# Kernel tuning notes

Hardware: AMD Instinct MI355X
Metric: run time of the kernel (lower is better)

## Reference

```python
import jax, jax.numpy as jnp
import numpy as np

D_MODEL, H, KV, D = 2048, 32, 8, 64
G = H // KV  # groups = 4
B, T = 1, 2048


def rotate_half(x):
    # interleaved rotation: (-x1, x0, -x3, x2, ...)
    x_even = x[..., ::2]
    x_odd = x[..., 1::2]
    return jnp.stack((-x_odd, x_even), axis=-1).reshape(x.shape)


def setup_inputs() -> dict:
    key = jax.random.key(0)
    kx, kq, kk, kv, ko = jax.random.split(key, 5)
    x = jax.random.normal(kx, (B, T, D_MODEL), dtype=jnp.float32)
    # RoPE frequency table: freqs[0]=cos, freqs[1]=sin, each [T, D] with pairwise-repeated angles
    inv_freq = 1.0 / (10000.0 ** (jnp.arange(0, D, 2, dtype=jnp.float32) / D))  # [D/2]
    angles = jnp.arange(T, dtype=jnp.float32)[:, None] * inv_freq[None, :]       # [T, D/2]
    angles = jnp.repeat(angles, 2, axis=-1)                                       # [T, D]
    freqs = jnp.stack((jnp.cos(angles), jnp.sin(angles)), axis=0)                 # [2, T, D]
    # causal mask, broadcastable to [B, H, T, T]
    mask = jnp.tril(jnp.ones((T, T), dtype=bool))[None, None]
    s = 0.02
    Wq = s * jax.random.normal(kq, (D_MODEL, H * D), dtype=jnp.float32)
    Wk = s * jax.random.normal(kk, (D_MODEL, KV * D), dtype=jnp.float32)
    Wv = s * jax.random.normal(kv, (D_MODEL, KV * D), dtype=jnp.float32)
    Wo = s * jax.random.normal(ko, (D_MODEL, D_MODEL), dtype=jnp.float32)
    return {"x": x, "freqs": freqs, "mask": mask, "Wq": Wq, "Wk": Wk, "Wv": Wv, "Wo": Wo}


def reference(x, freqs, mask, Wq, Wk, Wv, Wo):
    b, t, _ = x.shape
    Q = (x @ Wq).reshape(b, t, H, D)
    K = (x @ Wk).reshape(b, t, KV, D)
    V = (x @ Wv).reshape(b, t, KV, D)
    cos = freqs[0, :t][None, :, None, :]  # [1,T,1,D]
    sin = freqs[1, :t][None, :, None, :]
    Q = Q * cos + rotate_half(Q) * sin
    K = K * cos + rotate_half(K) * sin
    # GQA: repeat each KV head `groups` times along the head axis
    K = jnp.repeat(K, G, axis=2)  # [B,T,H,D]
    V = jnp.repeat(V, G, axis=2)
    scale = D ** -0.5
    scores = jnp.einsum('bqhd,bkhd->bhqk', Q, K) * scale  # [B,H,T,T]
    scores = jnp.where(mask, scores, -jnp.inf)
    attn = jax.nn.softmax(scores, axis=-1)  # dropout=0.0 (eval) -> identity
    out = jnp.einsum('bhqk,bkhd->bqhd', attn, V).reshape(b, t, H * D)
    return out @ Wo
```

## Files before the change

### kernel.cpp

```cpp
#include <hip/hip_runtime.h>
#include <hip/hip_bf16.h>

#define T_SEQ  2048
#define DMODEL 2048
#define NH     32
#define NKV    8
#define HD     64

typedef __attribute__((ext_vector_type(8))) short bf16x8;
typedef __attribute__((ext_vector_type(4))) short bf16x4;
typedef __attribute__((ext_vector_type(4))) float f32x4;

__device__ __forceinline__ unsigned short f2bf(float f) {
    unsigned int u = __float_as_uint(f);
    return (unsigned short)((u + 0x7FFFu + ((u >> 16) & 1u)) >> 16);
}
__device__ __forceinline__ float bf2f(unsigned short b) {
    return __uint_as_float(((unsigned int)b) << 16);
}
__device__ __forceinline__ unsigned int pk2bf(float a, float b) {
    float2 f; f.x = a; f.y = b;
    __hip_bfloat162 h = __float22bfloat162_rn(f);
    union { __hip_bfloat162 h; unsigned int u; } cv; cv.h = h;
    return cv.u;
}
__device__ __forceinline__ int is_bf16(const void* __restrict__ freqs) {
    return ((const unsigned int*)freqs)[0] != 0x3F800000u;
}
__device__ __forceinline__ float ldf(const void* __restrict__ p, size_t i, int bf) {
    return bf ? bf2f(((const unsigned short*)p)[i]) : ((const float*)p)[i];
}

__device__ __forceinline__ void gload_lds16(const void* g, void* l) {
    __builtin_amdgcn_global_load_lds(
        (const __attribute__((address_space(1))) void*)g,
        (__attribute__((address_space(3))) void*)l, 16, 0, 0);
}

__global__ __launch_bounds__(256) void prep_kernel(const void* __restrict__ x,
                                                   const void* __restrict__ Wq,
                                                   const void* __restrict__ Wk,
                                                   const void* __restrict__ Wv,
                                                   unsigned short* __restrict__ xb,
                                                   unsigned short* __restrict__ WqT,
                                                   unsigned short* __restrict__ WkT,
                                                   unsigned short* __restrict__ WvT,
                                                   const void* __restrict__ freqs) {
    const int bf = is_bf16(freqs);
    const int t  = threadIdx.x;
    const int z  = blockIdx.z;
    if (z == 3) {
        const int r0 = blockIdx.y * 64, c0 = blockIdx.x * 64;
#pragma unroll
        for (int it = 0; it < 16; ++it) {
            int e = t + it * 256;
            size_t idx = (size_t)(r0 + (e >> 6)) * DMODEL + c0 + (e & 63);
            xb[idx] = bf ? ((const unsigned short*)x)[idx] : f2bf(((const float*)x)[idx]);
        }
        return;
    }
    const void* W; unsigned short* Wt; int N;
    if (z == 0)      { W = Wq; Wt = WqT; N = 2048; }
    else if (z == 1) { if (blockIdx.x >= 8) return; W = Wk; Wt = WkT; N = 512; }
    else             { if (blockIdx.x >= 8) return; W = Wv; Wt = WvT; N = 512; }
    __shared__ unsigned short Tl[64][65];
    const int n0 = blockIdx.x * 64, k0 = blockIdx.y * 64;
#pragma unroll
    for (int it = 0; it < 16; ++it) {
        int e = t + it * 256;
        int r = e >> 6, c = e & 63;
        Tl[r][c] = bf ? ((const unsigned short*)W)[(size_t)(k0 + r) * N + n0 + c]
                      : f2bf(((const float*)W)[(size_t)(k0 + r) * N + n0 + c]);
    }
    __syncthreads();
#pragma unroll
    for (int it = 0; it < 16; ++it) {
        int e = t + it * 256;
        int r = e >> 6, c = e & 63;
        Wt[(size_t)(n0 + r) * DMODEL + k0 + c] = Tl[c][r];
    }
}

__global__ __launch_bounds__(256) void trans_one(const void* __restrict__ W,
                                                 unsigned short* __restrict__ Wt,
                                                 const void* __restrict__ freqs) {
    const int bf = is_bf16(freqs);
    __shared__ unsigned short Tl[64][65];
    const int t = threadIdx.x;
    const int n0 = blockIdx.x * 64, k0 = blockIdx.y * 64;
#pragma unroll
    for (int it = 0; it < 16; ++it) {
        int e = t + it * 256;
        int r = e >> 6, c = e & 63;
        Tl[r][c] = bf ? ((const unsigned short*)W)[(size_t)(k0 + r) * DMODEL + n0 + c]
                      : f2bf(((const float*)W)[(size_t)(k0 + r) * DMODEL + n0 + c]);
    }
    __syncthreads();
#pragma unroll
    for (int it = 0; it < 16; ++it) {
        int e = t + it * 256;
        int r = e >> 6, c = e & 63;
        Wt[(size_t)(n0 + r) * DMODEL + k0 + c] = Tl[c][r];
    }
}

template <int WM, int WN>
__device__ __forceinline__ void gemm_core(const unsigned short* __restrict__ A,
                                          const unsigned short* __restrict__ Bt,
                                          int K, int bm, int bn,
                                          f32x4 (&acc)[WM][WN]) {
    constexpr int BM = 32 * WM;
    constexpr int BN = 32 * WN;
    constexpr int AG = BM / 32;
    constexpr int BG = BN / 32;
    __shared__ unsigned short As[2 * BM * 64];
    __shared__ unsigned short Bs[2 * BN * 64];

    const int t    = threadIdx.x;
    const int w    = t >> 6;
    const int lane = t & 63;
    const int wm   = w & 1, wn = w >> 1;
    const int m0   = wm * WM * 16;
    const int n0   = wn * WN * 16;
    const int lrow = lane & 15;
    const int quad = lane >> 4;

    const int l3    = (lane & 7) ^ ((lane >> 3) & 7);
    const int srow  = lane >> 3;
    const int selem = l3 * 8;
    const int ps0 = (quad) ^ (lrow & 7);
    const int ps1 = (4 + quad) ^ (lrow & 7);

#pragma unroll
    for (int i = 0; i < WM; ++i)
#pragma unroll
        for (int j = 0; j < WN; ++j) acc[i][j] = (f32x4){0.f, 0.f, 0.f, 0.f};

#pragma unroll
    for (int it = 0; it < AG; ++it) {
        const int g = w * AG + it;
        gload_lds16(&A[(size_t)(bm + g * 8 + srow) * K + selem], &As[g * 512]);
    }
#pragma unroll
    for (int it = 0; it < BG; ++it) {
        const int g = w * BG + it;
        gload_lds16(&Bt[(size_t)(bn + g * 8 + srow) * K + selem], &Bs[g * 512]);
    }
    __syncthreads();

    const int nk = K >> 6;
    for (int ki = 0; ki < nk; ++ki) {
        const int buf = ki & 1;
        if (ki + 1 < nk) {
            const int k0 = (ki + 1) * 64;
#pragma unroll
            for (int it = 0; it < AG; ++it) {
                const int g = w * AG + it;
                gload_lds16(&A[(size_t)(bm + g * 8 + srow) * K + k0 + selem],
                            &As[(buf ^ 1) * (BM * 64) + g * 512]);
            }
#pragma unroll
            for (int it = 0; it < BG; ++it) {
                const int g = w * BG + it;
                gload_lds16(&Bt[(size_t)(bn + g * 8 + srow) * K + k0 + selem],
                            &Bs[(buf ^ 1) * (BN * 64) + g * 512]);
            }
        }
        bf16x8 af[WM][2], bfr[WN][2];
#pragma unroll
        for (int i = 0; i < WM; ++i) {
            const int row = m0 + i * 16 + lrow;
            af[i][0] = *(const bf16x8*)&As[buf * (BM * 64) + row * 64 + ps0 * 8];
            af[i][1] = *(const bf16x8*)&As[buf * (BM * 64) + row * 64 + ps1 * 8];
        }
#pragma unroll
        for (int j = 0; j < WN; ++j) {
            const int row = n0 + j * 16 + lrow;
            bfr[j][0] = *(const bf16x8*)&Bs[buf * (BN * 64) + row * 64 + ps0 * 8];
            bfr[j][1] = *(const bf16x8*)&Bs[buf * (BN * 64) + row * 64 + ps1 * 8];
        }
#pragma unroll
        for (int kk = 0; kk < 2; ++kk)
#pragma unroll
            for (int i = 0; i < WM; ++i)
#pragma unroll
                for (int j = 0; j < WN; ++j)
                    acc[i][j] = __builtin_amdgcn_mfma_f32_16x16x32_bf16(af[i][kk], bfr[j][kk], acc[i][j], 0, 0, 0);
        __syncthreads();
    }
}

__global__ __launch_bounds__(256) void gemm_mfma(const unsigned short* __restrict__ A,
                                                 const unsigned short* __restrict__ Bt,
                                                 void* __restrict__ C,
                                                 int N, int K,
                                                 const void* __restrict__ freqs) {
    f32x4 acc[2][4];
    const int bm = blockIdx.y * 64, bn = blockIdx.x * 128;
    gemm_core<2, 4>(A, Bt, K, bm, bn, acc);

    const int t = threadIdx.x, w = t >> 6, lane = t & 63;
    const int m0 = (w & 1) * 32, n0 = (w >> 1) * 64;
    const int lrow = lane & 15, quad = lane >> 4;
    const int cbf = is_bf16(freqs);
#pragma unroll
    for (int i = 0; i < 2; ++i)
#pragma unroll
        for (int j = 0; j < 4; ++j)
#pragma unroll
            for (int r = 0; r < 4; ++r) {
                int row = bm + m0 + i * 16 + quad * 4 + r;
                int col = bn + n0 + j * 16 + lrow;
                size_t idx = (size_t)row * N + col;
                float v = acc[i][j][r];
                if (cbf) ((unsigned short*)C)[idx] = f2bf(v);
                else     ((float*)C)[idx] = v;
            }
}

__global__ __launch_bounds__(256) void gemm_qkv(const unsigned short* __restrict__ A,
                                                const unsigned short* __restrict__ Bt,
                                                unsigned short* __restrict__ Qb,
                                                unsigned short* __restrict__ Kb,
                                                unsigned short* __restrict__ Vt_g) {
    f32x4 acc[2][4];
    const int bm = blockIdx.y * 64, bn = blockIdx.x * 128;
    gemm_core<2, 4>(A, Bt, DMODEL, bm, bn, acc);

    const int t = threadIdx.x, w = t >> 6, lane = t & 63;
    const int m0 = (w & 1) * 32, n0 = (w >> 1) * 64;
    const int lrow = lane & 15, quad = lane >> 4;
#pragma unroll
    for (int i = 0; i < 2; ++i)
#pragma unroll
        for (int j = 0; j < 4; ++j)
#pragma unroll
            for (int r = 0; r < 4; ++r) {
                int row = bm + m0 + i * 16 + quad * 4 + r;
                int col = bn + n0 + j * 16 + lrow;
                unsigned short v = f2bf(acc[i][j][r]);
                if (col < 2048)      Qb[(size_t)row * 2048 + col] = v;
                else if (col < 2560) Kb[(size_t)row * 512 + (col - 2048)] = v;
                else                 Vt_g[(size_t)(col - 2560) * T_SEQ + row] = v;
            }
}

__global__ void rope_kernel(unsigned short* __restrict__ Qb, unsigned short* __restrict__ Kb,
                            const void* __restrict__ freqs) {
    const int bf = is_bf16(freqs);
    int idx = blockIdx.x * blockDim.x + threadIdx.x;
    const int nq = T_SEQ * NH * 32;
    unsigned short* X; int nh; float scale; int li;
    if (idx < nq) { X = Qb; nh = NH; scale = 0.125f; li = idx; }
    else          { X = Kb; nh = NKV; scale = 1.0f; li = idx - nq;
                    if (li >= T_SEQ * NKV * 32) return; }
    int i = li & 31;
    int h = (li >> 5) % nh;
    int t = li / (nh * 32);
    float c = ldf(freqs, (size_t)t * 64 + 2 * i, bf);
    float s = ldf(freqs, (size_t)T_SEQ * 64 + (size_t)t * 64 + 2 * i, bf);
    int base = (t * nh + h) * HD + 2 * i;
    float x0 = bf2f(X[base]), x1 = bf2f(X[base + 1]);
    X[base]     = f2bf((x0 * c - x1 * s) * scale);
    X[base + 1] = f2bf((x1 * c + x0 * s) * scale);
}

__global__ __launch_bounds__(256) void attn_kernel(const unsigned short* __restrict__ Qb,
                                                   const unsigned short* __restrict__ Kb,
                                                   const unsigned short* __restrict__ Vt_g,
                                                   unsigned short* __restrict__ AO,
                                                   unsigned short* __restrict__ arena,
                                                   float* __restrict__ lpart) {
    __shared__ unsigned short Kf[2][8 * 64 * 8];
    __shared__ unsigned short Vf[2][8 * 64 * 8];

    const int t    = threadIdx.x;
    const int w    = t >> 6;
    const int lane = t & 63;
    const int lrow = lane & 15;
    const int quad = lane >> 4;
    const int hp   = blockIdx.y;
    const int kvh  = hp >> 1;
    const int h0   = kvh * 4 + (hp & 1) * 2;
    const int bxr  = 71 - (int)blockIdx.x;

    int qt, j, s;
    if (bxr < 8)       { qt = bxr; j = 0; s = 1; }
    else if (bxr < 24) { qt = 8 + ((bxr - 8) >> 1); j = (bxr - 8) & 1; s = 2; }
    else               { int e = bxr - 24; qt = 16 + e / 3; j = e % 3; s = 3; }
    const int n    = qt + 1;
    const int base = n / s, rem = n % s;
    const int nch  = base + (j < rem ? 1 : 0);
    const int cs   = j * base + (j < rem ? j : rem);
    const int q0   = qt * 64;
    const int koff = cs * 64;
    const bool mask_last = (cs + nch - 1) == qt;

    bf16x8 q_frag[2][2];
#pragma unroll
    for (int hh = 0; hh < 2; ++hh) {
        const unsigned short* qp = Qb + (size_t)(q0 + w * 16 + lrow) * (NH * HD) + (h0 + hh) * HD;
        q_frag[hh][0] = *(const bf16x8*)&qp[quad * 8];
        q_frag[hh][1] = *(const bf16x8*)&qp[32 + quad * 8];
    }

    const int    krow = 16 * w + lrow;
    const size_t vrow = (size_t)(kvh * HD + 16 * w + lrow) * T_SEQ;

    union U8 { bf16x8 v; bf16x4 hh[2]; unsigned short s[8]; unsigned int u32[4]; };

    bf16x8 kpre[2];
    bf16x4 vpre[2][2];
#pragma unroll
    for (int i = 0; i < 2; ++i) {
        kpre[i] = *(const bf16x8*)&Kb[(size_t)(koff + krow) * (NKV * HD) + kvh * HD + i * 32 + quad * 8];
        vpre[i][0] = *(const bf16x4*)&Vt_g[vrow + koff + i * 32 + quad * 4];
        vpre[i][1] = *(const bf16x4*)&Vt_g[vrow + koff + i * 32 + 16 + quad * 4];
    }
#pragma unroll
    for (int i = 0; i < 2; ++i) {
        *(bf16x8*)&Kf[0][((2 * w + i) * 64 + lane) * 8] = kpre[i];
        U8 u; u.hh[0] = vpre[i][0]; u.hh[1] = vpre[i][1];
        *(bf16x8*)&Vf[0][((2 * w + i) * 64 + lane) * 8] = u.v;
    }

    float l_s[2] = {0.0f, 0.0f};
    f32x4 oacc[2][4];
#pragma unroll
    for (int hh = 0; hh < 2; ++hh)
#pragma unroll
        for (int nc = 0; nc < 4; ++nc) oacc[hh][nc] = (f32x4){0.f, 0.f, 0.f, 0.f};

    for (int c = 0; c < nch; ++c) {
        __syncthreads();
        const int buf = c & 1;
        const bool pre = (c + 1 < nch);
        if (pre) {
            const int kb2 = koff + (c + 1) * 64;
#pragma unroll
            for (int i = 0; i < 2; ++i) {
                kpre[i] = *(const bf16x8*)&Kb[(size_t)(kb2 + krow) * (NKV * HD) + kvh * HD + i * 32 + quad * 8];
                vpre[i][0] = *(const bf16x4*)&Vt_g[vrow + kb2 + i * 32 + quad * 4];
                vpre[i][1] = *(const bf16x4*)&Vt_g[vrow + kb2 + i * 32 + 16 + quad * 4];
            }
        }

        f32x4 sacc[2][4];
#pragma unroll
        for (int hh = 0; hh < 2; ++hh)
#pragma unroll
            for (int kc = 0; kc < 4; ++kc) sacc[hh][kc] = (f32x4){0.f, 0.f, 0.f, 0.f};
#pragma unroll
        for (int kh = 0; kh < 2; ++kh) {
#pragma unroll
            for (int kc = 0; kc < 4; ++kc) {
                bf16x8 kf = *(const bf16x8*)&Kf[buf][((kc * 2 + kh) * 64 + lane) * 8];
                sacc[0][kc] = __builtin_amdgcn_mfma_f32_16x16x32_bf16(kf, q_frag[0][kh], sacc[0][kc], 0, 0, 0);
                sacc[1][kc] = __builtin_amdgcn_mfma_f32_16x16x32_bf16(kf, q_frag[1][kh], sacc[1][kc], 0, 0, 0);
            }
        }

        if (c == nch - 1 && mask_last) {
            const int qrow  = q0 + w * 16 + lrow;
            const int kbase = koff + c * 64 + quad * 4;
#pragma unroll
            for (int kc = 0; kc < 4; ++kc)
#pragma unroll
                for (int r = 0; r < 4; ++r)
                    if (kbase + kc * 16 + r > qrow) { sacc[0][kc][r] = -INFINITY; sacc[1][kc][r] = -INFINITY; }
        }

        bf16x8 pf[2][2];
#pragma unroll
        for (int hh = 0; hh < 2; ++hh) {
            float rsum = 0.0f;
#pragma unroll
            for (int kc = 0; kc < 4; ++kc)
#pragma unroll
                for (int r = 0; r < 4; ++r) {
                    sacc[hh][kc][r] = __expf(sacc[hh][kc][r]);
                    rsum += sacc[hh][kc][r];
                }
            l_s[hh] += rsum;
#pragma unroll
            for (int kh = 0; kh < 2; ++kh) {
                U8 u;
                u.u32[0] = pk2bf(sacc[hh][2 * kh][0], sacc[hh][2 * kh][1]);
                u.u32[1] = pk2bf(sacc[hh][2 * kh][2], sacc[hh][2 * kh][3]);
                u.u32[2] = pk2bf(sacc[hh][2 * kh + 1][0], sacc[hh][2 * kh + 1][1]);
                u.u32[3] = pk2bf(sacc[hh][2 * kh + 1][2], sacc[hh][2 * kh + 1][3]);
                pf[hh][kh] = u.v;
            }
        }

#pragma unroll
        for (int kh = 0; kh < 2; ++kh) {
#pragma unroll
            for (int nc = 0; nc < 4; ++nc) {
                bf16x8 vu = *(const bf16x8*)&Vf[buf][((nc * 2 + kh) * 64 + lane) * 8];
                oacc[0][nc] = __builtin_amdgcn_mfma_f32_16x16x32_bf16(pf[0][kh], vu, oacc[0][nc], 0, 0, 0);
                oacc[1][nc] = __builtin_amdgcn_mfma_f32_16x16x32_bf16(pf[1][kh], vu, oacc[1][nc], 0, 0, 0);
            }
        }

        if (pre) {
#pragma unroll
            for (int i = 0; i < 2; ++i) {
                *(bf16x8*)&Kf[buf ^ 1][((2 * w + i) * 64 + lane) * 8] = kpre[i];
                U8 u; u.hh[0] = vpre[i][0]; u.hh[1] = vpre[i][1];
                *(bf16x8*)&Vf[buf ^ 1][((2 * w + i) * 64 + lane) * 8] = u.v;
            }
        }
    }

#pragma unroll
    for (int hh = 0; hh < 2; ++hh) {
        const int h = h0 + hh;
        float ls = l_s[hh];
        ls += __shfl_xor(ls, 16);
        ls += __shfl_xor(ls, 32);

        if (s == 1) {
            const float linv = 1.0f / ls;
            float l_o[4];
#pragma unroll
            for (int r = 0; r < 4; ++r)
                l_o[r] = __shfl(linv, (lane & 48) | (quad * 4 + r));
#pragma unroll
            for (int nc = 0; nc < 4; ++nc)
#pragma unroll
                for (int r = 0; r < 4; ++r) {
                    int row = q0 + w * 16 + quad * 4 + r;
                    AO[(size_t)row * (NH * HD) + h * HD + nc * 16 + lrow] = f2bf(oacc[hh][nc][r] * l_o[r]);
                }
        } else {
            if (quad == 0)
                lpart[(((size_t)h * 32 + qt) * 3 + j) * 64 + (w * 16 + lrow)] = ls;
            if (j == 0) {
#pragma unroll
                for (int nc = 0; nc < 4; ++nc)
#pragma unroll
                    for (int r = 0; r < 4; ++r) {
                        int row = q0 + w * 16 + quad * 4 + r;
                        AO[(size_t)row * (NH * HD) + h * HD + nc * 16 + lrow] = f2bf(oacc[hh][nc][r]);
                    }
            } else {
                const int slot = (qt < 16) ? (qt - 8) : (8 + (qt - 16) * 2 + (j - 1));
                unsigned short* ap = arena + ((size_t)h * 40 + slot) * 4096;
#pragma unroll
                for (int nc = 0; nc < 4; ++nc)
#pragma unroll
                    for (int r = 0; r < 4; ++r)
                        ap[(size_t)(w * 16 + quad * 4 + r) * 64 + nc * 16 + lrow] = f2bf(oacc[hh][nc][r]);
            }
        }
    }
}

__global__ __launch_bounds__(256) void combine_kernel(unsigned short* __restrict__ AO,
                                                      const unsigned short* __restrict__ arena,
                                                      const float* __restrict__ lpart) {
    int idx = blockIdx.x * 256 + threadIdx.x;
    int row1 = idx >> 11;
    int col  = idx & 2047;
    int qt   = 8 + (row1 >> 6);
    int r    = row1 & 63;
    int h    = col >> 6;
    int d    = col & 63;
    int s    = (qt < 16) ? 2 : 3;

    size_t aoidx = (size_t)(512 + row1) * 2048 + col;
    float o = bf2f(AO[aoidx]);
    float l = lpart[(((size_t)h * 32 + qt) * 3 + 0) * 64 + r];
#pragma unroll
    for (int j = 1; j < 3; ++j) {
        if (j >= s) break;
        int slot = (qt < 16) ? (qt - 8) : (8 + (qt - 16) * 2 + (j - 1));
        o += bf2f(arena[((size_t)h * 40 + slot) * 4096 + (size_t)r * 64 + d]);
        l += lpart[(((size_t)h * 32 + qt) * 3 + j) * 64 + r];
    }
    AO[aoidx] = f2bf(o / l);
}

extern "C" void kernel_launch(void* const* d_in, const int* in_sizes, int n_in,
                              void* d_out, int out_size, void* d_ws, size_t ws_size,
                              hipStream_t stream) {
    const void* x     = d_in[0];
    const void* freqs = d_in[1];
    const void* Wq = d_in[3];
    const void* Wk = d_in[4];
    const void* Wv = d_in[5];
    const void* Wo = d_in[6];

    char* ws = (char*)d_ws;
    unsigned short* Qb   = (unsigned short*)(ws);
    unsigned short* Kb   = (unsigned short*)(ws + (8u  << 20));
    unsigned short* Vt_g = (unsigned short*)(ws + (10u << 20));
    unsigned short* xb   = (unsigned short*)(ws + (12u << 20));
    unsigned short* WT3  = (unsigned short*)(ws + (20u << 20));
    unsigned short* WkT  = WT3 + (size_t)2048 * 2048;
    unsigned short* WvT  = WT3 + (size_t)2560 * 2048;
    unsigned short* arena = (unsigned short*)(ws + (28u << 20));
    float*          lprt  = (float*)(ws + (38u << 20));
    unsigned short* AOb  = xb;

    prep_kernel<<<dim3(32, 32, 4), 256, 0, stream>>>(x, Wq, Wk, Wv, xb, WT3, WkT, WvT, freqs);

    gemm_qkv<<<dim3(3072 / 128, T_SEQ / 64), 256, 0, stream>>>(xb, WT3, Qb, Kb, Vt_g);

    rope_kernel<<<(T_SEQ * (NH + NKV) * 32) / 256, 256, 0, stream>>>(Qb, Kb, freqs);

    trans_one<<<dim3(32, 32), 256, 0, stream>>>(Wo, WT3, freqs);

    attn_kernel<<<dim3(72, 16), 256, 0, stream>>>(Qb, Kb, Vt_g, AOb, arena, lprt);

    combine_kernel<<<(1536 * 2048) / 256, 256, 0, stream>>>(AOb, arena, lprt);

    gemm_mfma<<<dim3(DMODEL / 128, T_SEQ / 64), 256, 0, stream>>>(
        AOb, WT3, d_out, DMODEL, DMODEL, freqs);
}
```

Before: 267.3 us.

## Vectorize prep, rope and combine kernels; raise wave priority around MFMA blocks

The x conversion in prep, the RoPE kernel and the split-combine kernel now handle 8 bf16 elements per thread with 16-byte loads and stores instead of scalar accesses, and their launch grids shrink to match. This is meant to cut memory-instruction count and uncoalesced traffic in these bandwidth-bound helper kernels. The attention kernel also wraps its two MFMA loops in s_setprio(1)/s_setprio(0) so waves issuing matrix ops get scheduling priority over waves doing softmax or loads. The combine kernel now multiplies by a reciprocal instead of dividing.

```diff
diff --git a/kernel.cpp b/kernel.cpp
--- a/kernel.cpp
+++ b/kernel.cpp
@@ -52,10 +52,19 @@
     if (z == 3) {
         const int r0 = blockIdx.y * 64, c0 = blockIdx.x * 64;
 #pragma unroll
-        for (int it = 0; it < 16; ++it) {
+        for (int it = 0; it < 2; ++it) {
             int e = t + it * 256;
-            size_t idx = (size_t)(r0 + (e >> 6)) * DMODEL + c0 + (e & 63);
-            xb[idx] = bf ? ((const unsigned short*)x)[idx] : f2bf(((const float*)x)[idx]);
+            int r = e >> 3, c8 = (e & 7) * 8;
+            size_t idx = (size_t)(r0 + r) * DMODEL + c0 + c8;
+            if (bf) {
+                *(bf16x8*)&xb[idx] = *(const bf16x8*)&((const unsigned short*)x)[idx];
+            } else {
+                union { bf16x8 v; unsigned short s[8]; } u;
+                const float* xf = (const float*)x;
+#pragma unroll
+                for (int p = 0; p < 8; ++p) u.s[p] = f2bf(xf[idx + p]);
+                *(bf16x8*)&xb[idx] = u.v;
+            }
         }
         return;
     }
@@ -249,20 +258,28 @@
                             const void* __restrict__ freqs) {
     const int bf = is_bf16(freqs);
     int idx = blockIdx.x * blockDim.x + threadIdx.x;
-    const int nq = T_SEQ * NH * 32;
+    const int nq8 = T_SEQ * NH * 8;
     unsigned short* X; int nh; float scale; int li;
-    if (idx < nq) { X = Qb; nh = NH; scale = 0.125f; li = idx; }
-    else          { X = Kb; nh = NKV; scale = 1.0f; li = idx - nq;
-                    if (li >= T_SEQ * NKV * 32) return; }
-    int i = li & 31;
-    int h = (li >> 5) % nh;
-    int t = li / (nh * 32);
-    float c = ldf(freqs, (size_t)t * 64 + 2 * i, bf);
-    float s = ldf(freqs, (size_t)T_SEQ * 64 + (size_t)t * 64 + 2 * i, bf);
-    int base = (t * nh + h) * HD + 2 * i;
-    float x0 = bf2f(X[base]), x1 = bf2f(X[base + 1]);
-    X[base]     = f2bf((x0 * c - x1 * s) * scale);
-    X[base + 1] = f2bf((x1 * c + x0 * s) * scale);
+    if (idx < nq8) { X = Qb; nh = NH; scale = 0.125f; li = idx; }
+    else           { X = Kb; nh = NKV; scale = 1.0f; li = idx - nq8;
+                     if (li >= T_SEQ * NKV * 8) return; }
+    int d8 = li & 7;
+    int h  = (li >> 3) % nh;
+    int t  = li / (nh * 8);
+    int dbase = d8 * 8;
+    size_t base = ((size_t)t * nh + h) * HD + dbase;
+    union { bf16x8 v; unsigned short s[8]; } u;
+    u.v = *(bf16x8*)&X[base];
+#pragma unroll
+    for (int p = 0; p < 4; ++p) {
+        int d = dbase + 2 * p;
+        float c = ldf(freqs, (size_t)t * 64 + d, bf);
+        float s = ldf(freqs, (size_t)(T_SEQ * 64) + (size_t)t * 64 + d, bf);
+        float x0 = bf2f(u.s[2 * p]), x1 = bf2f(u.s[2 * p + 1]);
+        u.s[2 * p]     = f2bf((x0 * c - x1 * s) * scale);
+        u.s[2 * p + 1] = f2bf((x1 * c + x0 * s) * scale);
+    }
+    *(bf16x8*)&X[base] = u.v;
 }
 
 __global__ __launch_bounds__(256) void attn_kernel(const unsigned short* __restrict__ Qb,
@@ -350,6 +367,7 @@
         for (int hh = 0; hh < 2; ++hh)
 #pragma unroll
             for (int kc = 0; kc < 4; ++kc) sacc[hh][kc] = (f32x4){0.f, 0.f, 0.f, 0.f};
+        __builtin_amdgcn_s_setprio(1);
 #pragma unroll
         for (int kh = 0; kh < 2; ++kh) {
 #pragma unroll
@@ -359,6 +377,7 @@
                 sacc[1][kc] = __builtin_amdgcn_mfma_f32_16x16x32_bf16(kf, q_frag[1][kh], sacc[1][kc], 0, 0, 0);
             }
         }
+        __builtin_amdgcn_s_setprio(0);
 
         if (c == nch - 1 && mask_last) {
             const int qrow  = q0 + w * 16 + lrow;
@@ -393,6 +412,7 @@
             }
         }
 
+        __builtin_amdgcn_s_setprio(1);
 #pragma unroll
         for (int kh = 0; kh < 2; ++kh) {
 #pragma unroll
@@ -402,6 +422,7 @@
                 oacc[1][nc] = __builtin_amdgcn_mfma_f32_16x16x32_bf16(pf[1][kh], vu, oacc[1][nc], 0, 0, 0);
             }
         }
+        __builtin_amdgcn_s_setprio(0);
 
         if (pre) {
 #pragma unroll
@@ -461,25 +482,34 @@
                                                       const unsigned short* __restrict__ arena,
                                                       const float* __restrict__ lpart) {
     int idx = blockIdx.x * 256 + threadIdx.x;
-    int row1 = idx >> 11;
-    int col  = idx & 2047;
+    int row1 = idx >> 8;
+    int c8   = (idx & 255) * 8;
     int qt   = 8 + (row1 >> 6);
     int r    = row1 & 63;
-    int h    = col >> 6;
-    int d    = col & 63;
+    int h    = c8 >> 6;
+    int d    = c8 & 63;
     int s    = (qt < 16) ? 2 : 3;
 
-    size_t aoidx = (size_t)(512 + row1) * 2048 + col;
-    float o = bf2f(AO[aoidx]);
+    size_t aoidx = (size_t)(512 + row1) * 2048 + c8;
+    union U { bf16x8 v; unsigned short sh[8]; } o, a;
+    o.v = *(const bf16x8*)&AO[aoidx];
+    float ov[8];
+#pragma unroll
+    for (int p = 0; p < 8; ++p) ov[p] = bf2f(o.sh[p]);
     float l = lpart[(((size_t)h * 32 + qt) * 3 + 0) * 64 + r];
 #pragma unroll
     for (int j = 1; j < 3; ++j) {
         if (j >= s) break;
         int slot = (qt < 16) ? (qt - 8) : (8 + (qt - 16) * 2 + (j - 1));
-        o += bf2f(arena[((size_t)h * 40 + slot) * 4096 + (size_t)r * 64 + d]);
+        a.v = *(const bf16x8*)&arena[((size_t)h * 40 + slot) * 4096 + (size_t)r * 64 + d];
+#pragma unroll
+        for (int p = 0; p < 8; ++p) ov[p] += bf2f(a.sh[p]);
         l += lpart[(((size_t)h * 32 + qt) * 3 + j) * 64 + r];
     }
-    AO[aoidx] = f2bf(o / l);
+    const float linv = 1.0f / l;
+#pragma unroll
+    for (int p = 0; p < 8; ++p) o.sh[p] = f2bf(ov[p] * linv);
+    *(bf16x8*)&AO[aoidx] = o.v;
 }
 
 extern "C" void kernel_launch(void* const* d_in, const int* in_sizes, int n_in,
@@ -508,13 +538,13 @@
 
     gemm_qkv<<<dim3(3072 / 128, T_SEQ / 64), 256, 0, stream>>>(xb, WT3, Qb, Kb, Vt_g);
 
-    rope_kernel<<<(T_SEQ * (NH + NKV) * 32) / 256, 256, 0, stream>>>(Qb, Kb, freqs);
+    rope_kernel<<<(T_SEQ * (NH + NKV) * 8) / 256, 256, 0, stream>>>(Qb, Kb, freqs);
 
     trans_one<<<dim3(32, 32), 256, 0, stream>>>(Wo, WT3, freqs);
 
     attn_kernel<<<dim3(72, 16), 256, 0, stream>>>(Qb, Kb, Vt_g, AOb, arena, lprt);
 
-    combine_kernel<<<(1536 * 2048) / 256, 256, 0, stream>>>(AOb, arena, lprt);
+    combine_kernel<<<(1536 * 2048) / 8 / 256, 256, 0, stream>>>(AOb, arena, lprt);
 
     gemm_mfma<<<dim3(DMODEL / 128, T_SEQ / 64), 256, 0, stream>>>(
         AOb, WT3, d_out, DMODEL, DMODEL, freqs);
```

Result: no change. 270.5 us (+1.2%).
